# Performance work log

Measured on AMD Instinct MI355X. Metric: run time of the kernel, lower is better.

## Reference

```python
import jax, jax.numpy as jnp
import numpy as np

MARGIN = 1.0


def setup_inputs() -> dict:
    key = jax.random.key(0)
    k1, k2, k3 = jax.random.split(key, 3)
    B, D, C = 16384, 256, 2000
    pred_embedding = jax.random.normal(k1, (B, D), dtype=jnp.float32)
    batch_label = jax.random.randint(k2, (B,), 0, C, dtype=jnp.int64)
    train_classes = jnp.arange(C, dtype=jnp.int64)
    train_sig = jax.random.normal(k3, (D, C), dtype=jnp.float32)
    return {
        "pred_embedding": pred_embedding,
        "batch_label": batch_label,
        "train_classes": train_classes,
        "train_sig": train_sig,
    }


def reference(pred_embedding, batch_label, train_classes, train_sig):
    # scores[j, k] = <pred_embedding[j], train_sig[:, train_classes[k]]>
    # Single GEMM replaces the per-pair dot-product loops.
    sig_cols = train_sig[:, train_classes]            # [D, C]
    scores = jnp.einsum("bd,dc->bc", pred_embedding, sig_cols)  # [B, C]
    # ground-truth class score per row: <XW_j, train_sig[:, y_j]>
    gt = jnp.einsum("bd,db->b", pred_embedding, train_sig[:, batch_label])  # [B]
    # exclude the class equal to the row label
    mask = (train_classes[None, :] != batch_label[:, None])  # [B, C] bool
    hinge = jnp.maximum(MARGIN + scores - gt[:, None], 0.0)
    loss = jnp.sum(jnp.where(mask, hinge, 0.0))
    return loss
```

## Files before the change

kernel.cpp:

```cpp
#include <hip/hip_runtime.h>

#define B_SZ 16384
#define D_SZ 256
#define C_SZ 2000
#define C_PAD 2048
#define MARGIN_F 1.0f
#define NBLK 1024

typedef float floatx16 __attribute__((ext_vector_type(16)));

__device__ inline void gld_lds16(const void* g, void* l) {
  __builtin_amdgcn_global_load_lds(
      (const __attribute__((address_space(1))) void*)g,
      (__attribute__((address_space(3))) void*)l, 16, 0, 0);
}


__device__ inline int2 pack8_fp8(const float* v) {
  int lo = __builtin_amdgcn_cvt_pk_fp8_f32(v[0], v[1], 0, false);
  lo = __builtin_amdgcn_cvt_pk_fp8_f32(v[2], v[3], lo, true);
  int hi = __builtin_amdgcn_cvt_pk_fp8_f32(v[4], v[5], 0, false);
  hi = __builtin_amdgcn_cvt_pk_fp8_f32(v[6], v[7], hi, true);
  return make_int2(lo, hi);
}
__device__ inline float rt_fp8(float x) {
  int p = __builtin_amdgcn_cvt_pk_fp8_f32(x, x, 0, false);
  return __builtin_amdgcn_cvt_f32_fp8(p, 0);
}
__device__ inline void unpack4_fp8(int w, float* o) {
  o[0] = __builtin_amdgcn_cvt_f32_fp8(w, 0);
  o[1] = __builtin_amdgcn_cvt_f32_fp8(w, 1);
  o[2] = __builtin_amdgcn_cvt_f32_fp8(w, 2);
  o[3] = __builtin_amdgcn_cvt_f32_fp8(w, 3);
}

__global__ __launch_bounds__(256) void sigq_kernel(
    const float* __restrict__ sig, char* __restrict__ sigq,
    float* __restrict__ out) {
  int t = blockIdx.x * 256 + threadIdx.x;
  if (t == 0) out[0] = 0.f;
  int ln = t & 63, ks = (t >> 6) & 15, ct = t >> 10;
  int col = ct * 32 + (ln & 31);
  int kb = ks * 16 + (ln >> 5) * 8;
  float v[8];
#pragma unroll
  for (int j = 0; j < 8; j++)
    v[j] = (col < C_SZ) ? sig[(size_t)(kb + j) * C_SZ + col] : 0.f;
  *(int2*)(sigq + (size_t)t * 8) = pack8_fp8(v);
}

__global__ __launch_bounds__(256) void prep_kernel(
    const float* __restrict__ pred, const char* __restrict__ sigq,
    const int* __restrict__ label, char* __restrict__ predq,
    float* __restrict__ gt) {
  __shared__ float ldsP[16][260];
  int bid = (int)blockIdx.x;
  int tid = threadIdx.x;
  int lane = tid & 63;
  int w = tid >> 6;
  int tile = bid >> 1;
  int rhi = (bid & 1) * 16;
#pragma unroll
  for (int it = 0; it < 4; it++) {
    int idx = it * 1024 + tid * 4;
    int r = idx >> 8, c = idx & 255;
    *(float4*)&ldsP[r][c] = *(const float4*)(pred + (size_t)(bid * 16 + r) * D_SZ + c);
  }
  __syncthreads();
#pragma unroll
  for (int it = 0; it < 2; it++) {
    int ch = it * 256 + tid;
    int ri = ch & 15;
    int ks = (ch >> 4) & 15;
    int kh = ch >> 8;
    int kb = ks * 16 + kh * 8;
    int ln = kh * 32 + rhi + ri;
    float v[8];
#pragma unroll
    for (int j = 0; j < 8; j++) v[j] = ldsP[ri][kb + j];
    *(int2*)(predq + ((size_t)(tile * 16 + ks) * 64 + ln) * 8) = pack8_fp8(v);
  }
  int l = lane & 31;
  int half = lane >> 5;
#pragma unroll
  for (int it = 0; it < 2; it++) {
    int r = w * 4 + it * 2 + half;
    int row = bid * 16 + r;
    int lbl = label[row];
    int ltile = lbl >> 5, l5 = lbl & 31;
    int ks = l >> 1, kh = l & 1;
    int2 p8 = *(const int2*)(sigq +
        (((size_t)(ltile * 16 + ks) * 64) + kh * 32 + l5) * 8);
    float sv[8];
    unpack4_fp8(p8.x, sv);
    unpack4_fp8(p8.y, sv + 4);
    float s = 0.f;
#pragma unroll
    for (int j = 0; j < 8; j++)
      s += rt_fp8(ldsP[r][l * 8 + j]) * sv[j];
#pragma unroll
    for (int off = 16; off > 0; off >>= 1) s += __shfl_down(s, off, 32);
    if (l == 0) gt[row] = s;
  }
}

__global__ __launch_bounds__(256) void mfma_fused_kernel(
    const char* __restrict__ predq, const char* __restrict__ sigq,
    const float* __restrict__ gt, float* __restrict__ out) {
  __shared__ char Bs[4096 * 8];
  __shared__ float red[4];
  int tid = threadIdx.x;
  int lane = tid & 63;
  int w = tid >> 6;
  int kh = lane >> 5, lm = lane & 31;
  int bid = (int)blockIdx.x;
  int i = bid >> 3;
  int rsb = (bid & 7) * 8 + (i & 7);
  int cg = i >> 3;

#pragma unroll
  for (int s = 0; s < 8; s++) {
    int q0 = s * 256 + w * 64;
    gld_lds16(sigq + ((size_t)cg * 2048 + q0 + lane) * 16, (void*)(Bs + (size_t)q0 * 16));
  }

  long afr[2][16];
#pragma unroll
  for (int rt = 0; rt < 2; rt++)
#pragma unroll
    for (int ks = 0; ks < 16; ks++)
      afr[rt][ks] = *(const long*)(predq +
          (((size_t)(rsb * 8 + w * 2 + rt) * 16 + ks) * 64 + lane) * 8);

  float mgv[2][16];
#pragma unroll
  for (int rt = 0; rt < 2; rt++)
#pragma unroll
    for (int reg = 0; reg < 16; reg++) {
      int row = rsb * 256 + w * 64 + rt * 32 + (reg & 3) + 8 * (reg >> 2) + 4 * kh;
      mgv[rt][reg] = MARGIN_F - gt[row];
    }
  __syncthreads();

  float sum = 0.f;
#pragma unroll
  for (int ct = 0; ct < 4; ct++) {
    floatx16 acc0 = {}, acc1 = {};
#pragma unroll
    for (int ks = 0; ks < 16; ks++) {
      long b = *(const long*)(Bs + (size_t)((ct * 16 + ks) * 64 + lane) * 8);
      acc0 = __builtin_amdgcn_mfma_f32_32x32x16_fp8_fp8(afr[0][ks], b, acc0, 0, 0, 0);
      acc1 = __builtin_amdgcn_mfma_f32_32x32x16_fp8_fp8(afr[1][ks], b, acc1, 0, 0, 0);
    }
    int col = cg * 128 + ct * 32 + lm;
    float keep = (col < C_SZ) ? 1.f : 0.f;
#pragma unroll
    for (int reg = 0; reg < 16; reg++) {
      sum += keep * fmaxf(acc0[reg] + mgv[0][reg], 0.f);
      sum += keep * fmaxf(acc1[reg] + mgv[1][reg], 0.f);
    }
  }
#pragma unroll
  for (int off = 32; off > 0; off >>= 1) sum += __shfl_down(sum, off, 64);
  if (lane == 0) red[w] = sum;
  __syncthreads();
  if (tid == 0)
    atomicAdd(out, red[0] + red[1] + red[2] + red[3]
                   - (float)B_SZ * MARGIN_F / (float)NBLK);
}

extern "C" void kernel_launch(void* const* d_in, const int* in_sizes, int n_in,
                              void* d_out, int out_size, void* d_ws, size_t ws_size,
                              hipStream_t stream) {
  const float* pred  = (const float*)d_in[0];
  const int*   label = (const int*)d_in[1];
  const float* sig   = (const float*)d_in[3];
  float* out = (float*)d_out;

  float* gt    = (float*)d_ws;
  char*  predq = (char*)d_ws + (128 << 10);
  char*  sigq  = (char*)d_ws + (128 << 10) + (4 << 20);

  sigq_kernel<<<256, 256, 0, stream>>>(sig, sigq, out);
  prep_kernel<<<1024, 256, 0, stream>>>(pred, sigq, label, predq, gt);
  mfma_fused_kernel<<<NBLK, 256, 0, stream>>>(predq, sigq, gt, out);
}
```

Before: 96.96 us.

## Use 32x32x64 scaled fp8 MFMA and stage gt through LDS

Replaces the sixteen 32x32x16 fp8 MFMAs per tile with four 32x32x64 scaled MFMAs (unit scales), regrouping the A and B fragment loads into 8-int vectors over the existing packed layout. Ground-truth scores are loaded into LDS with an async global-to-LDS copy and read per row in the epilogue instead of being held in 32 registers. Launch bounds now request 4 blocks per CU to cut register pressure and raise occupancy. The K-grouping of the fragments must match the wider instruction's operand layout, which is a correctness risk.

```diff
diff --git a/kernel.cpp b/kernel.cpp
--- a/kernel.cpp
+++ b/kernel.cpp
@@ -8,6 +8,7 @@
 #define NBLK 1024
 
 typedef float floatx16 __attribute__((ext_vector_type(16)));
+typedef int   intx8    __attribute__((ext_vector_type(8)));
 
 __device__ inline void gld_lds16(const void* g, void* l) {
   __builtin_amdgcn_global_load_lds(
@@ -72,9 +73,9 @@
     int ch = it * 256 + tid;
     int ri = ch & 15;
     int ks = (ch >> 4) & 15;
-    int kh = ch >> 8;
-    int kb = ks * 16 + kh * 8;
-    int ln = kh * 32 + rhi + ri;
+    int khh = ch >> 8;
+    int kb = ks * 16 + khh * 8;
+    int ln = khh * 32 + rhi + ri;
     float v[8];
 #pragma unroll
     for (int j = 0; j < 8; j++) v[j] = ldsP[ri][kb + j];
@@ -88,9 +89,9 @@
     int row = bid * 16 + r;
     int lbl = label[row];
     int ltile = lbl >> 5, l5 = lbl & 31;
-    int ks = l >> 1, kh = l & 1;
+    int ks = l >> 1, khh = l & 1;
     int2 p8 = *(const int2*)(sigq +
-        (((size_t)(ltile * 16 + ks) * 64) + kh * 32 + l5) * 8);
+        (((size_t)(ltile * 16 + ks) * 64) + khh * 32 + l5) * 8);
     float sv[8];
     unpack4_fp8(p8.x, sv);
     unpack4_fp8(p8.y, sv + 4);
@@ -104,10 +105,11 @@
   }
 }
 
-__global__ __launch_bounds__(256) void mfma_fused_kernel(
+__global__ __launch_bounds__(256, 4) void mfma_fused_kernel(
     const char* __restrict__ predq, const char* __restrict__ sigq,
     const float* __restrict__ gt, float* __restrict__ out) {
   __shared__ char Bs[4096 * 8];
+  __shared__ float gtl[256];
   __shared__ float red[4];
   int tid = threadIdx.x;
   int lane = tid & 63;
@@ -123,41 +125,49 @@
     int q0 = s * 256 + w * 64;
     gld_lds16(sigq + ((size_t)cg * 2048 + q0 + lane) * 16, (void*)(Bs + (size_t)q0 * 16));
   }
+  if (w == 0)
+    gld_lds16((const char*)gt + (size_t)rsb * 1024 + (size_t)lane * 16, (void*)gtl);
 
-  long afr[2][16];
+  union frag8 { long l[4]; intx8 v; };
+  frag8 a8[2][4];
 #pragma unroll
-  for (int rt = 0; rt < 2; rt++)
+  for (int rt = 0; rt < 2; rt++) {
+    const char* abase = predq + (size_t)(rsb * 8 + w * 2 + rt) * 8192
+                              + (size_t)(kh * 1024 + lm * 8);
 #pragma unroll
-    for (int ks = 0; ks < 16; ks++)
-      afr[rt][ks] = *(const long*)(predq +
-          (((size_t)(rsb * 8 + w * 2 + rt) * 16 + ks) * 64 + lane) * 8);
-
-  float mgv[2][16];
+    for (int ks = 0; ks < 4; ks++)
 #pragma unroll
-  for (int rt = 0; rt < 2; rt++)
-#pragma unroll
-    for (int reg = 0; reg < 16; reg++) {
-      int row = rsb * 256 + w * 64 + rt * 32 + (reg & 3) + 8 * (reg >> 2) + 4 * kh;
-      mgv[rt][reg] = MARGIN_F - gt[row];
-    }
+      for (int g = 0; g < 4; g++)
+        a8[rt][ks].l[g] = *(const long*)(abase + ks * 2048 + g * 256);
+  }
   __syncthreads();
 
+  volatile const float* vgt = gtl;
   float sum = 0.f;
 #pragma unroll
   for (int ct = 0; ct < 4; ct++) {
     floatx16 acc0 = {}, acc1 = {};
+    const char* bbase = Bs + ct * 8192 + kh * 1024 + lm * 8;
 #pragma unroll
-    for (int ks = 0; ks < 16; ks++) {
-      long b = *(const long*)(Bs + (size_t)((ct * 16 + ks) * 64 + lane) * 8);
-      acc0 = __builtin_amdgcn_mfma_f32_32x32x16_fp8_fp8(afr[0][ks], b, acc0, 0, 0, 0);
-      acc1 = __builtin_amdgcn_mfma_f32_32x32x16_fp8_fp8(afr[1][ks], b, acc1, 0, 0, 0);
+    for (int ks = 0; ks < 4; ks++) {
+      frag8 b8;
+#pragma unroll
+      for (int g = 0; g < 4; g++)
+        b8.l[g] = *(const long*)(bbase + ks * 2048 + g * 256);
+      acc0 = __builtin_amdgcn_mfma_scale_f32_32x32x64_f8f6f4(
+          a8[0][ks].v, b8.v, acc0, 0, 0, 0, 127, 0, 127);
+      acc1 = __builtin_amdgcn_mfma_scale_f32_32x32x64_f8f6f4(
+          a8[1][ks].v, b8.v, acc1, 0, 0, 0, 127, 0, 127);
     }
     int col = cg * 128 + ct * 32 + lm;
     float keep = (col < C_SZ) ? 1.f : 0.f;
 #pragma unroll
     for (int reg = 0; reg < 16; reg++) {
-      sum += keep * fmaxf(acc0[reg] + mgv[0][reg], 0.f);
-      sum += keep * fmaxf(acc1[reg] + mgv[1][reg], 0.f);
+      int rl = (reg & 3) + 8 * (reg >> 2) + 4 * kh;
+      float mg0 = MARGIN_F - vgt[w * 64 + rl];
+      float mg1 = MARGIN_F - vgt[w * 64 + 32 + rl];
+      sum += keep * fmaxf(acc0[reg] + mg0, 0.f);
+      sum += keep * fmaxf(acc1[reg] + mg1, 0.f);
     }
   }
 #pragma unroll
```

New measurement: 124.4 us. +28.3%, slower.
